# Optimization experiments

Hardware: AMD Instinct MI355X
Metric: run time of the kernel (lower is better)

## Reference

```python
import jax, jax.numpy as jnp
import numpy as np

LOG_HALF = float(np.log(0.5))  # log_g(0) = log(relu(0)+0.5) = log(0.5)

def log_g(x):
    # log of g(x) = where(x>=0, x+0.5, sigmoid(x))
    return jnp.where(x >= 0.0, jnp.log(jnp.maximum(x, 0.0) + 0.5), -jax.nn.softplus(-x))

def setup_inputs() -> dict:
    key = jax.random.key(0)
    k1, k2, k3, k4 = jax.random.split(key, 4)
    B, T, D, E = 4, 4096, 1024, 1536
    x = jax.random.normal(k1, (B, T, D), dtype=jnp.float32)
    W_f = jax.random.normal(k2, (2 * E, D), dtype=jnp.float32) * 0.02
    b_f = jax.random.normal(k3, (2 * E,), dtype=jnp.float32) * 0.02
    W_down = jax.random.normal(k4, (D, E), dtype=jnp.float32) * 0.02
    return {"x": x, "W_f": W_f, "b_f": b_f, "W_down": W_down}

def reference(x, W_f, b_f, W_down):
    B, T, D = x.shape
    E = W_down.shape[1]
    # fused input projection, split into gate pre-act k and candidate pre-act h_x
    kz, h_x = jnp.split(jnp.einsum('btd,ed->bte', x, W_f) + b_f, 2, axis=-1)
    log_z = -jax.nn.softplus(-kz)          # log sigmoid(k)
    log_coeffs = -jax.nn.softplus(kz)      # log (1 - sigmoid(k))
    log_tilde_h = log_g(h_x)
    # prepend initial log hidden state log_g(0) = log 0.5
    log_h0 = jnp.full((B, 1, E), LOG_HALF, dtype=x.dtype)
    log_values = jnp.concatenate([log_h0, log_tilde_h + log_z], axis=1)  # (B, T+1, E)
    # a_star = pad(cumsum(log_coeffs), one zero row at front along time)
    a_star = jnp.concatenate(
        [jnp.zeros((B, 1, E), dtype=x.dtype), jnp.cumsum(log_coeffs, axis=1)], axis=1)
    log_h = a_star + jax.lax.cumlogsumexp(log_values - a_star, axis=1)
    h = jnp.exp(log_h)[:, 1:]              # (B, T, E)
    return jnp.einsum('bte,de->btd', h, W_down)
```

## Files before the change

kernel.cpp:

```cpp
#include <hip/hip_runtime.h>
#include <hip/hip_bf16.h>
#include <stdint.h>


typedef __bf16 bf16x8 __attribute__((ext_vector_type(8)));
typedef float  f32x4  __attribute__((ext_vector_type(4)));

__device__ __forceinline__ uint16_t f32_to_bf16(float f) {
  union { float f; uint32_t u; } v; v.f = f;
  uint32_t r = (v.u + 0x7FFFu + ((v.u >> 16) & 1u)) >> 16;
  return (uint16_t)r;
}
__device__ __forceinline__ float bf16_to_f32(uint16_t u) {
  union { uint32_t u; float f; } v; v.u = ((uint32_t)u) << 16;
  return v.f;
}

__device__ __forceinline__ void gload_lds16(const uint16_t* g, uint16_t* l) {
  __builtin_amdgcn_global_load_lds(
      (__attribute__((address_space(1))) void*)(g),
      (__attribute__((address_space(3))) void*)(l), 16, 0, 0);
}

__device__ __forceinline__ void cast4(const float* s, uint16_t* d, int j) {
  float4 v = reinterpret_cast<const float4*>(s)[j];
  ushort4 o;
  o.x = f32_to_bf16(v.x); o.y = f32_to_bf16(v.y);
  o.z = f32_to_bf16(v.z); o.w = f32_to_bf16(v.w);
  reinterpret_cast<ushort4*>(d)[j] = o;
}

__global__ __launch_bounds__(256) void cast_all(
    const float* __restrict__ x,   uint16_t* __restrict__ x_bf,
    const float* __restrict__ W_f, uint16_t* __restrict__ Wf_bf,
    const float* __restrict__ b_f, float* __restrict__ bias_p,
    const float* __restrict__ W_d, uint16_t* __restrict__ Wd_bf) {
  const int stride = gridDim.x * blockDim.x;
  const int gid = blockIdx.x * blockDim.x + threadIdx.x;
  if (gid < 3072)
    bias_p[gid] = b_f[(gid & 1) ? 1536 + (gid >> 1) : (gid >> 1)];
  for (int i = gid; i < 4194304; i += stride) cast4(x, x_bf, i);
  for (int i = gid; i < 786432; i += stride) {
    const int r = i >> 8, cg = i & 255;
    const int rp = (r < 1536) ? (r << 1) : (((r - 1536) << 1) | 1);
    float4 v = reinterpret_cast<const float4*>(W_f)[i];
    ushort4 o;
    o.x = f32_to_bf16(v.x); o.y = f32_to_bf16(v.y);
    o.z = f32_to_bf16(v.z); o.w = f32_to_bf16(v.w);
    reinterpret_cast<ushort4*>(Wf_bf)[rp * 256 + cg] = o;
  }
  for (int i = gid; i < 393216; i += stride) cast4(W_d, Wd_bf, i);
}

template <int OUT_BF16_BIAS>
__global__ __launch_bounds__(512, 2) void gemm256(
    const uint16_t* __restrict__ A, const uint16_t* __restrict__ Bt,
    const float* __restrict__ bias, void* __restrict__ Cout,
    int M, int N, int K) {
  __shared__ alignas(16) uint16_t lds[4 * 16384];

  const int tid  = threadIdx.x;
  const int wave = tid >> 6;
  const int lane = tid & 63;
  const int wr = wave >> 2;
  const int wc = wave & 3;

  const int bid = (int)blockIdx.x;
  const int xq  = bid & 7;
  const int j   = bid >> 3;
  const int pi  = xq + ((j >> 3) << 3);
  const int q   = j & 7;
  const int mt  = ((pi & 31) << 1) + (q >> 2);
  const int nt  = ((pi >> 5) << 2) + (q & 3);
  const int m0  = mt << 8;
  const int n0  = nt << 8;

  const int NT = K >> 5;

  const int srow = wave * 16 + (lane >> 2);
  const int skg  = (lane & 3) ^ ((lane >> 3) & 3);
  const uint16_t* Ag0 = A  + (size_t)(m0 + srow) * K + skg * 8;
  const uint16_t* Ag1 = A  + (size_t)(m0 + 128 + srow) * K + skg * 8;
  const uint16_t* Bg0 = Bt + (size_t)(n0 + srow) * K + skg * 8;
  const uint16_t* Bg1 = Bt + (size_t)(n0 + 128 + srow) * K + skg * 8;
  const int sdw = wave * 512;

  const int kgq = (lane >> 4) ^ ((lane >> 1) & 3);
  const int rA = (wr * 128 + (lane & 15)) * 32 + kgq * 8;
  const int rB = (wc * 64  + (lane & 15)) * 32 + kgq * 8;

  f32x4 acc[8][4] = {};

#pragma unroll
  for (int tt = 0; tt < 3; ++tt) {
    uint16_t* sb = &lds[tt * 16384];
    gload_lds16(Ag0 + tt * 32, sb + sdw);
    gload_lds16(Ag1 + tt * 32, sb + 4096 + sdw);
    gload_lds16(Bg0 + tt * 32, sb + 8192 + sdw);
    gload_lds16(Bg1 + tt * 32, sb + 12288 + sdw);
  }

  for (int u = 0; u < NT; ++u) {
    const uint16_t* Ab = &lds[(u & 3) * 16384 + rA];
    const uint16_t* Bb = &lds[(u & 3) * 16384 + 8192 + rB];
    const int us = (u + 3 < NT) ? (u + 3) : (NT - 1);
    uint16_t* sb = &lds[((u + 3) & 3) * 16384];
    const size_t kofs = (size_t)us * 32;

    asm volatile("s_waitcnt vmcnt(8)" ::: "memory");
    __builtin_amdgcn_s_barrier();

    bf16x8 af0[4], af1[4], bfr[4];
#pragma unroll
    for (int m = 0; m < 4; ++m) af0[m] = *reinterpret_cast<const bf16x8*>(Ab + m * 512);
#pragma unroll
    for (int n = 0; n < 4; ++n) bfr[n] = *reinterpret_cast<const bf16x8*>(Bb + n * 512);
    gload_lds16(Ag0 + kofs, sb + sdw);
    gload_lds16(Ag1 + kofs, sb + 4096 + sdw);
    __builtin_amdgcn_sched_barrier(0);
    __builtin_amdgcn_s_barrier();
    asm volatile("s_waitcnt lgkmcnt(0)" ::: "memory");
    __builtin_amdgcn_sched_barrier(0);
    __builtin_amdgcn_s_setprio(1);
#pragma unroll
    for (int m = 0; m < 4; ++m)
#pragma unroll
      for (int n = 0; n < 4; ++n)
        acc[m][n] = __builtin_amdgcn_mfma_f32_16x16x32_bf16(bfr[n], af0[m], acc[m][n], 0, 0, 0);
    __builtin_amdgcn_s_setprio(0);
    __builtin_amdgcn_sched_barrier(0);

#pragma unroll
    for (int m = 0; m < 4; ++m) af1[m] = *reinterpret_cast<const bf16x8*>(Ab + (m + 4) * 512);
    gload_lds16(Bg0 + kofs, sb + 8192 + sdw);
    gload_lds16(Bg1 + kofs, sb + 12288 + sdw);
    __builtin_amdgcn_sched_barrier(0);
    __builtin_amdgcn_s_barrier();
    asm volatile("s_waitcnt lgkmcnt(0)" ::: "memory");
    __builtin_amdgcn_sched_barrier(0);
    __builtin_amdgcn_s_setprio(1);
#pragma unroll
    for (int m = 0; m < 4; ++m)
#pragma unroll
      for (int n = 0; n < 4; ++n)
        acc[m + 4][n] = __builtin_amdgcn_mfma_f32_16x16x32_bf16(bfr[n], af1[m], acc[m + 4][n], 0, 0, 0);
    __builtin_amdgcn_s_setprio(0);
    __builtin_amdgcn_sched_barrier(0);
  }
  asm volatile("s_waitcnt vmcnt(0)" ::: "memory");

  const int r0 = m0 + wr * 128 + (lane & 15);
  const int cb = n0 + wc * 64 + (lane >> 4) * 4;
  if constexpr (OUT_BF16_BIAS) {
    uint16_t* C = (uint16_t*)Cout;
#pragma unroll
    for (int m = 0; m < 8; ++m) {
      const int row = r0 + m * 16;
#pragma unroll
      for (int n = 0; n < 4; ++n) {
        const int col = cb + n * 16;
        ushort4 o;
        o.x = f32_to_bf16(acc[m][n][0] + bias[col + 0]);
        o.y = f32_to_bf16(acc[m][n][1] + bias[col + 1]);
        o.z = f32_to_bf16(acc[m][n][2] + bias[col + 2]);
        o.w = f32_to_bf16(acc[m][n][3] + bias[col + 3]);
        *reinterpret_cast<ushort4*>(&C[(size_t)row * N + col]) = o;
      }
    }
  } else {
    float* C = (float*)Cout;
#pragma unroll
    for (int m = 0; m < 8; ++m) {
      const int row = r0 + m * 16;
#pragma unroll
      for (int n = 0; n < 4; ++n) {
        const int col = cb + n * 16;
        float4 o;
        o.x = acc[m][n][0]; o.y = acc[m][n][1];
        o.z = acc[m][n][2]; o.w = acc[m][n][3];
        *reinterpret_cast<float4*>(&C[(size_t)row * N + col]) = o;
      }
    }
  }
}

__device__ __forceinline__ void gate_val(float kz, float hx, float& a, float& v) {
  float ek = __expf(-fabsf(kz));
  float r  = 1.0f / (1.0f + ek);
  float z  = (kz >= 0.0f) ? r : ek * r;
  a        = (kz >= 0.0f) ? ek * r : r;
  float g;
  if (hx >= 0.0f) {
    g = hx + 0.5f;
  } else {
    float eh = __expf(hx);
    g = eh / (1.0f + eh);
  }
  v = z * g;
}

__device__ __forceinline__ void gate_from_u32(uint32_t u, float& a, float& v) {
  float kz = bf16_to_f32((uint16_t)(u & 0xFFFFu));
  float hx = bf16_to_f32((uint16_t)(u >> 16));
  gate_val(kz, hx, a, v);
}

__global__ __launch_bounds__(256) void scan_pass1(
    const uint16_t* __restrict__ proj, float* __restrict__ Ac,
    float* __restrict__ Vc, int T, int E, int CH, int L) {
  const int e = blockIdx.x * 256 + threadIdx.x;
  const int c = blockIdx.y;
  const int b = blockIdx.z;
  const int N1 = 2 * E;
  const uint16_t* p = proj + (size_t)(b * T + c * L) * N1 + 2 * e;
  float A = 1.0f, V = 0.0f;
#pragma unroll 4
  for (int t = 0; t < L; ++t) {
    float a, v; gate_from_u32(*reinterpret_cast<const uint32_t*>(p), a, v);
    A *= a;
    V = a * V + v;
    p += N1;
  }
  const size_t idx = ((size_t)(b * CH + c)) * E + e;
  Ac[idx] = A; Vc[idx] = V;
}

__global__ __launch_bounds__(256) void scan_pass3(
    const uint16_t* __restrict__ proj, const float* __restrict__ Ac,
    const float* __restrict__ Vc, uint16_t* __restrict__ hout,
    int T, int E, int CH, int L) {
  const int e = blockIdx.x * 256 + threadIdx.x;
  const int c = blockIdx.y;
  const int b = blockIdx.z;
  const int N1 = 2 * E;
  float h = 0.5f;
  for (int cc = 0; cc < c; ++cc) {
    const size_t idx = ((size_t)(b * CH + cc)) * E + e;
    h = Ac[idx] * h + Vc[idx];
  }
  const uint16_t* p = proj + (size_t)(b * T + c * L) * N1 + 2 * e;
  uint16_t* o = hout + (size_t)(b * T + c * L) * E + e;
#pragma unroll 4
  for (int t = 0; t < L; ++t) {
    float a, v; gate_from_u32(*reinterpret_cast<const uint32_t*>(p), a, v);
    h = a * h + v;
    *o = f32_to_bf16(h);
    p += N1; o += E;
  }
}

extern "C" void kernel_launch(void* const* d_in, const int* in_sizes, int n_in,
                              void* d_out, int out_size, void* d_ws, size_t ws_size,
                              hipStream_t stream) {
  const float* x   = (const float*)d_in[0];
  const float* W_f = (const float*)d_in[1];
  const float* b_f = (const float*)d_in[2];
  const float* W_d = (const float*)d_in[3];
  const int Bb = 4, T = 4096, D = 1024, E = 1536;
  const int M = Bb * T;
  const int N1 = 2 * E;
  const int CH = 64, L = T / CH;

  char* w = (char*)d_ws;
  uint16_t* x_bf  = (uint16_t*)w; w += (size_t)M * D * 2;
  uint16_t* Wf_bf = (uint16_t*)w; w += (size_t)N1 * D * 2;
  uint16_t* Wd_bf = (uint16_t*)w; w += (size_t)D * E * 2;
  uint16_t* proj  = (uint16_t*)w; w += (size_t)M * N1 * 2;
  uint16_t* h_bf  = (uint16_t*)w; w += (size_t)M * E * 2;
  float* Ac     = (float*)w; w += (size_t)Bb * CH * E * 4;
  float* Vc     = (float*)w; w += (size_t)Bb * CH * E * 4;
  float* bias_p = (float*)w; w += (size_t)N1 * 4;

  cast_all<<<2048, 256, 0, stream>>>(x, x_bf, W_f, Wf_bf, b_f, bias_p, W_d, Wd_bf);

  gemm256<1><<<(M / 256) * (N1 / 256), 512, 0, stream>>>(
      x_bf, Wf_bf, bias_p, proj, M, N1, D);

  scan_pass1<<<dim3(E / 256, CH, Bb), 256, 0, stream>>>(proj, Ac, Vc, T, E, CH, L);
  scan_pass3<<<dim3(E / 256, CH, Bb), 256, 0, stream>>>(proj, Ac, Vc, h_bf, T, E, CH, L);

  gemm256<0><<<(M / 256) * (D / 256), 512, 0, stream>>>(
      h_bf, Wd_bf, nullptr, d_out, M, D, E);
}
```

Measured before the change: 283.7 us.

## Fuse scan pass1 chunk reduction into projection GEMM epilogue, double-buffer LDS

Removes the separate scan_pass1 kernel. Each projection GEMM block now rereads its just-written bf16 output tile from global memory (expected to be cache-resident) and computes per-chunk scan aggregates (A, V) for 4 chunks of 64 timesteps over 128 channels. The GEMM's LDS pipeline also shrinks from 4 stages to 2, with a full vmcnt(0) wait each iteration. This cuts LDS use but exposes more load latency in both GEMMs. The epilogue reads other threads' global writes after a barrier, which relies on memory visibility within the block.

```diff
diff --git a/kernel.cpp b/kernel.cpp
--- a/kernel.cpp
+++ b/kernel.cpp
@@ -20,6 +20,26 @@
   __builtin_amdgcn_global_load_lds(
       (__attribute__((address_space(1))) void*)(g),
       (__attribute__((address_space(3))) void*)(l), 16, 0, 0);
+}
+
+__device__ __forceinline__ void gate_val(float kz, float hx, float& a, float& v) {
+  float ek = __expf(-fabsf(kz));
+  float r  = 1.0f / (1.0f + ek);
+  float z  = (kz >= 0.0f) ? r : ek * r;
+  a        = (kz >= 0.0f) ? ek * r : r;
+  float g;
+  if (hx >= 0.0f) {
+    g = hx + 0.5f;
+  } else {
+    float eh = __expf(hx);
+    g = eh / (1.0f + eh);
+  }
+  v = z * g;
+}
+__device__ __forceinline__ void gate_from_u32(uint32_t u, float& a, float& v) {
+  float kz = bf16_to_f32((uint16_t)(u & 0xFFFFu));
+  float hx = bf16_to_f32((uint16_t)(u >> 16));
+  gate_val(kz, hx, a, v);
 }
 
 __device__ __forceinline__ void cast4(const float* s, uint16_t* d, int j) {
@@ -52,12 +72,13 @@
   for (int i = gid; i < 393216; i += stride) cast4(W_d, Wd_bf, i);
 }
 
-template <int OUT_BF16_BIAS>
+template <int OUT_BF16_BIAS, int FUSE_SCAN>
 __global__ __launch_bounds__(512, 2) void gemm256(
     const uint16_t* __restrict__ A, const uint16_t* __restrict__ Bt,
     const float* __restrict__ bias, void* __restrict__ Cout,
+    float* __restrict__ Ac, float* __restrict__ Vc,
     int M, int N, int K) {
-  __shared__ alignas(16) uint16_t lds[4 * 16384];
+  __shared__ alignas(16) uint16_t lds[2 * 16384];
 
   const int tid  = threadIdx.x;
   const int wave = tid >> 6;
@@ -91,23 +112,19 @@
 
   f32x4 acc[8][4] = {};
 
-#pragma unroll
-  for (int tt = 0; tt < 3; ++tt) {
-    uint16_t* sb = &lds[tt * 16384];
-    gload_lds16(Ag0 + tt * 32, sb + sdw);
-    gload_lds16(Ag1 + tt * 32, sb + 4096 + sdw);
-    gload_lds16(Bg0 + tt * 32, sb + 8192 + sdw);
-    gload_lds16(Bg1 + tt * 32, sb + 12288 + sdw);
-  }
+  gload_lds16(Ag0, &lds[sdw]);
+  gload_lds16(Ag1, &lds[4096 + sdw]);
+  gload_lds16(Bg0, &lds[8192 + sdw]);
+  gload_lds16(Bg1, &lds[12288 + sdw]);
 
   for (int u = 0; u < NT; ++u) {
-    const uint16_t* Ab = &lds[(u & 3) * 16384 + rA];
-    const uint16_t* Bb = &lds[(u & 3) * 16384 + 8192 + rB];
-    const int us = (u + 3 < NT) ? (u + 3) : (NT - 1);
-    uint16_t* sb = &lds[((u + 3) & 3) * 16384];
+    const uint16_t* Ab = &lds[(u & 1) * 16384 + rA];
+    const uint16_t* Bb = &lds[(u & 1) * 16384 + 8192 + rB];
+    const int us = (u + 1 < NT) ? (u + 1) : (NT - 1);
+    uint16_t* sb = &lds[((u + 1) & 1) * 16384];
     const size_t kofs = (size_t)us * 32;
 
-    asm volatile("s_waitcnt vmcnt(8)" ::: "memory");
+    asm volatile("s_waitcnt vmcnt(0)" ::: "memory");
     __builtin_amdgcn_s_barrier();
 
     bf16x8 af0[4], af1[4], bfr[4];
@@ -182,47 +199,29 @@
       }
     }
   }
-}
-
-__device__ __forceinline__ void gate_val(float kz, float hx, float& a, float& v) {
-  float ek = __expf(-fabsf(kz));
-  float r  = 1.0f / (1.0f + ek);
-  float z  = (kz >= 0.0f) ? r : ek * r;
-  a        = (kz >= 0.0f) ? ek * r : r;
-  float g;
-  if (hx >= 0.0f) {
-    g = hx + 0.5f;
-  } else {
-    float eh = __expf(hx);
-    g = eh / (1.0f + eh);
-  }
-  v = z * g;
-}
-
-__device__ __forceinline__ void gate_from_u32(uint32_t u, float& a, float& v) {
-  float kz = bf16_to_f32((uint16_t)(u & 0xFFFFu));
-  float hx = bf16_to_f32((uint16_t)(u >> 16));
-  gate_val(kz, hx, a, v);
-}
-
-__global__ __launch_bounds__(256) void scan_pass1(
-    const uint16_t* __restrict__ proj, float* __restrict__ Ac,
-    float* __restrict__ Vc, int T, int E, int CH, int L) {
-  const int e = blockIdx.x * 256 + threadIdx.x;
-  const int c = blockIdx.y;
-  const int b = blockIdx.z;
-  const int N1 = 2 * E;
-  const uint16_t* p = proj + (size_t)(b * T + c * L) * N1 + 2 * e;
-  float A = 1.0f, V = 0.0f;
-#pragma unroll 4
-  for (int t = 0; t < L; ++t) {
-    float a, v; gate_from_u32(*reinterpret_cast<const uint32_t*>(p), a, v);
-    A *= a;
-    V = a * V + v;
-    p += N1;
-  }
-  const size_t idx = ((size_t)(b * CH + c)) * E + e;
-  Ac[idx] = A; Vc[idx] = V;
+
+  if constexpr (FUSE_SCAN) {
+    asm volatile("s_waitcnt vmcnt(0)" ::: "memory");
+    __builtin_amdgcn_s_barrier();
+    const int cidx = tid >> 7;
+    const int el   = tid & 127;
+    const int b    = m0 >> 12;
+    const int c    = ((m0 & 4095) >> 6) + cidx;
+    const uint16_t* pr = (const uint16_t*)Cout +
+        (size_t)(m0 + cidx * 64) * N + n0 + 2 * el;
+    float Aa = 1.0f, Vv = 0.0f;
+#pragma unroll 8
+    for (int t = 0; t < 64; ++t) {
+      uint32_t u32 = *reinterpret_cast<const uint32_t*>(pr);
+      float a, v; gate_from_u32(u32, a, v);
+      Aa *= a;
+      Vv = a * Vv + v;
+      pr += N;
+    }
+    const int E = N >> 1;
+    const size_t idx = ((size_t)(b * 64 + c)) * E + (n0 >> 1) + el;
+    Ac[idx] = Aa; Vc[idx] = Vv;
+  }
 }
 
 __global__ __launch_bounds__(256) void scan_pass3(
@@ -273,12 +272,11 @@
 
   cast_all<<<2048, 256, 0, stream>>>(x, x_bf, W_f, Wf_bf, b_f, bias_p, W_d, Wd_bf);
 
-  gemm256<1><<<(M / 256) * (N1 / 256), 512, 0, stream>>>(
-      x_bf, Wf_bf, bias_p, proj, M, N1, D);
-
-  scan_pass1<<<dim3(E / 256, CH, Bb), 256, 0, stream>>>(proj, Ac, Vc, T, E, CH, L);
+  gemm256<1, 1><<<(M / 256) * (N1 / 256), 512, 0, stream>>>(
+      x_bf, Wf_bf, bias_p, proj, Ac, Vc, M, N1, D);
+
   scan_pass3<<<dim3(E / 256, CH, Bb), 256, 0, stream>>>(proj, Ac, Vc, h_bf, T, E, CH, L);
 
-  gemm256<0><<<(M / 256) * (D / 256), 512, 0, stream>>>(
-      h_bf, Wd_bf, nullptr, d_out, M, D, E);
-}
+  gemm256<0, 0><<<(M / 256) * (D / 256), 512, 0, stream>>>(
+      h_bf, Wd_bf, nullptr, d_out, nullptr, nullptr, M, D, E);
+}
```

After: 319.7 us. 1.13x slower.
